# Performance work log

Measured on AMD Instinct MI355X. Metric: run time of the kernel, lower is better.

The kernel has to match this reference:

```python
import jax, jax.numpy as jnp
import numpy as np

NUM_HEADS = 16


def setup_inputs() -> dict:
    key = jax.random.key(0)
    ks = jax.random.split(key, 8)
    b, n, m, L, d = 2, 1024, 4, 1024, 1024
    x = jax.random.normal(ks[0], (b, n, d), dtype=jnp.float32)
    context = jax.random.normal(ks[1], (b, m, L, d), dtype=jnp.float32)
    doc_similarities = jax.random.normal(ks[2], (b, m), dtype=jnp.float32)
    mask = jnp.ones((b, n), dtype=bool)
    context_mask = jnp.ones((b, m, L), dtype=bool)
    Wq = jax.random.normal(ks[3], (d, d), dtype=jnp.float32) * 0.02
    Wkv = jax.random.normal(ks[4], (d, 2 * d), dtype=jnp.float32) * 0.02
    Wout = jax.random.normal(ks[5], (d, d), dtype=jnp.float32) * 0.02
    bout = jnp.zeros((d,), dtype=jnp.float32)
    beta = jnp.ones((), dtype=jnp.float32)
    return {"x": x, "context": context, "doc_similarities": doc_similarities,
            "mask": mask, "context_mask": context_mask,
            "Wq": Wq, "Wkv": Wkv, "Wout": Wout, "bout": bout, "beta": beta}


def reference(x, context, doc_similarities, mask, context_mask, Wq, Wkv, Wout, bout, beta):
    b, n, d = x.shape
    h = NUM_HEADS
    hd = d // h
    _, m, L, _ = context.shape
    kv_len = m * L

    # q projection -> (b, h, n, hd)
    q = (x @ Wq).reshape(b, n, h, hd).transpose(0, 2, 1, 3)

    ctx = context.reshape(b, kv_len, d)
    cmask = context_mask.reshape(b, kv_len)

    # doc similarity bias, broadcast per-token within each doc, scaled by beta
    ds = jnp.repeat(doc_similarities[:, :, None], L, axis=-1).reshape(b, kv_len)
    ds = ds[:, None, None, :] * beta  # (b, 1, 1, kv_len)

    kv = ctx @ Wkv  # (b, kv_len, 2d)
    k, v = jnp.split(kv, 2, axis=-1)
    k = k.reshape(b, kv_len, h, hd).transpose(0, 2, 3, 1)  # (b, h, hd, kv_len)
    v = v.reshape(b, kv_len, h, hd).transpose(0, 2, 1, 3)  # (b, h, kv_len, hd)

    # NOTE: original scales by d**-0.5 (full model dim), not head_size**-0.5
    attention_pre_doc_sim = (q @ k) * (d ** -0.5)  # (b, h, n, kv_len)
    attention = attention_pre_doc_sim + ds

    # faithful mask path: multiply by cross mask, then map exact zeros to -inf
    cross_mask = mask[:, None, :, None] * cmask[:, None, None, :]  # (b,1,n,kv_len)
    attention = attention * cross_mask
    attention = jnp.where(attention == 0.0, -jnp.inf, attention)

    attention_weights = jax.nn.softmax(attention, axis=-1)
    # dropout_rate = 0.0 -> identity

    out = (attention_weights @ v).transpose(0, 2, 1, 3).reshape(b, n, d)
    out = out @ Wout + bout
    return out, attention_pre_doc_sim
```

## Files before the change

kernel.cpp:

```cpp
#include <hip/hip_runtime.h>
#include <cstdint>
#include <cstddef>

typedef unsigned short u16t;
typedef __attribute__((ext_vector_type(4))) float f32x4;
typedef __attribute__((ext_vector_type(4))) int i32x4;
typedef __attribute__((ext_vector_type(4))) unsigned int u32x4;
typedef __attribute__((ext_vector_type(8))) __bf16 bf16x8;
typedef __attribute__((ext_vector_type(4))) __bf16 bf16x4;
typedef __attribute__((ext_vector_type(8))) unsigned short u16x8;
typedef __attribute__((ext_vector_type(4))) unsigned short u16x4;

#define INFF __builtin_inff()

__device__ __forceinline__ u16t f2b(float f) {
  union { float f; unsigned u; } x; x.f = f;
  unsigned r = x.u + 0x7FFFu + ((x.u >> 16) & 1u);
  return (u16t)(r >> 16);
}

__device__ __forceinline__ void gload16(const u16t* g, u16t* l) {
  __builtin_amdgcn_global_load_lds((const __attribute__((address_space(1))) void*)g,
                                   (__attribute__((address_space(3))) void*)l, 16, 0, 0);
}

__global__ __launch_bounds__(256) void k_prep(const float* __restrict__ x,
                                              const float* __restrict__ ctx,
                                              u16t* __restrict__ x16,
                                              u16t* __restrict__ ctx16,
                                              const int* __restrict__ cmask,
                                              unsigned int* __restrict__ cmbits) {
  const int bx = blockIdx.x, tid = threadIdx.x;
  if (bx < 2048) {
    int i = bx * 256 + tid;
    f32x4 v = *(const f32x4*)(x + (size_t)i * 4);
    u16x4 o;
    o[0] = f2b(v[0]); o[1] = f2b(v[1]); o[2] = f2b(v[2]); o[3] = f2b(v[3]);
    *(u16x4*)(x16 + (size_t)i * 4) = o;
  } else if (bx < 10240) {
    int i = (bx - 2048) * 256 + tid;
    f32x4 v = *(const f32x4*)(ctx + (size_t)i * 4);
    u16x4 o;
    o[0] = f2b(v[0]); o[1] = f2b(v[1]); o[2] = f2b(v[2]); o[3] = f2b(v[3]);
    *(u16x4*)(ctx16 + (size_t)i * 4) = o;
  } else {
    int b = tid >> 7, wdi = tid & 127;
    const int* cp = cmask + b * 4096 + wdi * 32;
    unsigned int bits = 0;
#pragma unroll
    for (int i = 0; i < 32; ++i) bits |= (cp[i] != 0 ? 1u : 0u) << i;
    cmbits[tid] = bits;
  }
}

__global__ __launch_bounds__(256) void k_transpose_w3(const float* __restrict__ Wq,
                                                      const float* __restrict__ Wkv,
                                                      const float* __restrict__ Wout,
                                                      u16t* __restrict__ WqT,
                                                      u16t* __restrict__ WkvT,
                                                      u16t* __restrict__ WoutT) {
  __shared__ float tile[64 * 65];
  const int t = threadIdx.x;
  const int bxx = blockIdx.x;
  const float* src; u16t* dst; int C, cb;
  if (bxx < 16)      { src = Wq;   dst = WqT;   C = 1024; cb = bxx * 64; }
  else if (bxx < 48) { src = Wkv;  dst = WkvT;  C = 2048; cb = (bxx - 16) * 64; }
  else               { src = Wout; dst = WoutT; C = 1024; cb = (bxx - 48) * 64; }
  const int rb = blockIdx.y * 64;
#pragma unroll
  for (int it = 0; it < 4; ++it) {
    int c = it * 256 + t;
    int r = c >> 4, ch = c & 15;
    f32x4 v = *(const f32x4*)(src + (size_t)(rb + r) * C + cb + ch * 4);
    float* dp = &tile[r * 65 + ch * 4];
    dp[0] = v[0]; dp[1] = v[1]; dp[2] = v[2]; dp[3] = v[3];
  }
  __syncthreads();
#pragma unroll
  for (int it = 0; it < 2; ++it) {
    int c = it * 256 + t;
    int dr = c >> 3, ch = c & 7;
    u16x8 o;
#pragma unroll
    for (int i = 0; i < 8; ++i) o[i] = f2b(tile[(ch * 8 + i) * 65 + dr]);
    *(u16x8*)(dst + (size_t)(cb + dr) * 1024 + rb + ch * 8) = o;
  }
}

template <int MODE>
__global__ __launch_bounds__(256) void k_gemm_bt(const u16t* __restrict__ A,
                                                 const u16t* __restrict__ Bt,
                                                 void* __restrict__ C,
                                                 u16t* __restrict__ C2,
                                                 const float* __restrict__ bias,
                                                 float oscale,
                                                 int K, int lda, int ldb, int ldc, int nbx) {
  __shared__ u16t As[128 * 64];
  __shared__ u16t Bs[128 * 64];
  const int tid = threadIdx.x;
  const int lane = tid & 63, wid = tid >> 6;
  const int l16 = lane & 15, lg = lane >> 4;
  const int wr = wid >> 1, wc = wid & 1;
  const int g = blockIdx.x, per = gridDim.x >> 3;
  const int w = (g & 7) * per + (g >> 3);
  const int bx = w % nbx, by = w / nbx;
  const int brow = by * 128, bcol = bx * 128;
  const int sr = lane >> 3, chs = lane & 7;
  f32x4 acc[4][4] = {};

  for (int k0 = 0; k0 < K; k0 += 64) {
#pragma unroll
    for (int it = 0; it < 4; ++it) {
      int row = it * 32 + wid * 8 + sr;
      int ch = chs ^ (row & 7);
      gload16(A + (size_t)(brow + row) * lda + k0 + ch * 8, &As[it * 2048 + wid * 512]);
      gload16(Bt + (size_t)(bcol + row) * ldb + k0 + ch * 8, &Bs[it * 2048 + wid * 512]);
    }
    __syncthreads();
#pragma unroll
    for (int kk = 0; kk < 2; ++kk) {
      bf16x8 af[4], bfv[4];
#pragma unroll
      for (int mi = 0; mi < 4; ++mi) {
        int row = wr * 64 + mi * 16 + l16;
        int kch = (kk * 4 + lg) ^ (row & 7);
        af[mi] = *(const bf16x8*)(&As[row * 64 + kch * 8]);
      }
#pragma unroll
      for (int ni = 0; ni < 4; ++ni) {
        int row = wc * 64 + ni * 16 + l16;
        int kch = (kk * 4 + lg) ^ (row & 7);
        bfv[ni] = *(const bf16x8*)(&Bs[row * 64 + kch * 8]);
      }
#pragma unroll
      for (int mi = 0; mi < 4; ++mi)
#pragma unroll
        for (int ni = 0; ni < 4; ++ni)
          acc[mi][ni] = __builtin_amdgcn_mfma_f32_16x16x32_bf16(af[mi], bfv[ni], acc[mi][ni], 0, 0, 0);
    }
    __syncthreads();
  }

  if (MODE == 2 && bcol >= 1024) {
#pragma unroll
    for (int mi = 0; mi < 4; ++mi) {
#pragma unroll
      for (int ni = 0; ni < 4; ++ni) {
        int vcol = bcol - 1024 + wc * 64 + ni * 16 + l16;
        int h = vcol >> 6, hd = vcol & 63;
        int row0 = brow + wr * 64 + mi * 16 + lg * 4;
        int bb = row0 >> 12, pos = row0 & 4095;
        u16x4 o4;
#pragma unroll
        for (int j = 0; j < 4; ++j) o4[j] = f2b(acc[mi][ni][j]);
        *(u16x4*)(C2 + ((size_t)((bb * 16 + h) * 64 + hd)) * 4096 + pos) = o4;
      }
    }
    return;
  }
#pragma unroll
  for (int mi = 0; mi < 4; ++mi) {
#pragma unroll
    for (int ni = 0; ni < 4; ++ni) {
#pragma unroll
      for (int j = 0; j < 4; ++j) {
        size_t row = (size_t)brow + wr * 64 + mi * 16 + lg * 4 + j;
        int col = bcol + wc * 64 + ni * 16 + l16;
        float v = acc[mi][ni][j] * oscale;
        if (MODE == 1) {
          v += bias[col];
          __builtin_nontemporal_store(v, (float*)C + row * ldc + col);
        } else {
          ((u16t*)C)[row * ldc + col] = f2b(v);
        }
      }
    }
  }
}

__global__ __launch_bounds__(256) void k_attn(const u16t* __restrict__ k16,
                                              const u16t* __restrict__ vT16,
                                              const u16t* __restrict__ q16,
                                              const unsigned int* __restrict__ cmbits,
                                              const float* __restrict__ dsim,
                                              const float* __restrict__ beta_p,
                                              const int* __restrict__ mask,
                                              float* __restrict__ pre,
                                              u16t* __restrict__ O16) {
  __shared__ u16t Ks[2][128 * 64];
  __shared__ u16t Vs[2][64 * 128];
  __shared__ u16t Ps[4 * 16 * 128];

  const int tid = threadIdx.x;
  const int lane = tid & 63, wid = tid >> 6;
  const int l16 = lane & 15, lg = lane >> 4;
  const int g = blockIdx.x;
  const int w = (g & 7) * 64 + (g >> 3);
  const int nb = w & 15, hb = w >> 4;
  const int h = hb & 15, b = hb >> 4;
  const int qrow0 = nb * 64 + wid * 16;

  bf16x8 aq0, aq1;
  {
    const u16t* qp = q16 + (size_t)(b * 1024 + qrow0 + l16) * 1024 + h * 64 + lg * 8;
    aq0 = *(const bf16x8*)(qp);
    aq1 = *(const bf16x8*)(qp + 32);
  }
  const bool qm = mask[b * 1024 + qrow0 + l16] != 0;

  const float beta = beta_p[0];
  const float ds40 = dsim[b * 4 + 0] * beta, ds41 = dsim[b * 4 + 1] * beta;
  const float ds42 = dsim[b * 4 + 2] * beta, ds43 = dsim[b * 4 + 3] * beta;

  float mrow = -INFF, lsum = 0.f;
  f32x4 o[4] = {};

  const u16t* kbase = k16 + (size_t)b * 4096 * 1024 + (size_t)h * 64;
  const u16t* vbase = vT16 + (size_t)(b * 16 + h) * 64 * 4096;
  float* prerow = pre + (size_t)((b * 16 + h) * 1024 + qrow0 + l16) * 4096;
  const u32x4* cmw = (const u32x4*)(cmbits + b * 128);
  u16t* Pw = &Ps[wid * 2048];
  char* Pwb = (char*)Pw + l16 * 256;
  const int pswz = (l16 & 7) << 4;

  auto stage = [&](int bufi, int kv0s) {
    u16t* Kb = &Ks[bufi][wid * 2048];
    u16t* Vb = &Vs[bufi][wid * 2048];
#pragma unroll
    for (int it = 0; it < 4; ++it) {
      int row = wid * 32 + it * 8 + (lane >> 3);
      int ch = (lane & 7) ^ (row & 7);
      gload16(kbase + (size_t)(kv0s + row) * 1024 + ch * 8, Kb + it * 512);
    }
#pragma unroll
    for (int it = 0; it < 4; ++it) {
      int row = wid * 16 + it * 4 + (lane >> 4);
      int ch = (lane & 15) ^ (row & 7);
      gload16(vbase + (size_t)row * 4096 + kv0s + ch * 8, Vb + it * 512);
    }
  };

  u32x4 Wc = cmw[0];
  int cur = 0;
  stage(0, 0);
  __syncthreads();

  for (int t = 0; t < 32; ++t) {
    u32x4 Wn = Wc;
    if (t + 1 < 32) {
      Wn = cmw[t + 1];
      stage(cur ^ 1, (t + 1) * 128);
    }
    asm volatile("" ::: "memory");
    const u16t* Kc = &Ks[cur][0];
    const u16t* Vc = &Vs[cur][0];
    const int kv0 = t * 128;
    const int d = t >> 3;
    const float ds_t = (d & 1) ? ((d & 2) ? ds43 : ds41) : ((d & 2) ? ds42 : ds40);

    f32x4 s[8];
#pragma unroll
    for (int kb = 0; kb < 8; ++kb) {
      f32x4 acc = {0.f, 0.f, 0.f, 0.f};
      int row = kb * 16 + l16;
      bf16x8 bk0 = *(const bf16x8*)(&Kc[row * 64 + ((lg ^ (row & 7)) << 3)]);
      bf16x8 bk1 = *(const bf16x8*)(&Kc[row * 64 + (((4 + lg) ^ (row & 7)) << 3)]);
      acc = __builtin_amdgcn_mfma_f32_16x16x32_bf16(bk0, aq0, acc, 0, 0, 0);
      acc = __builtin_amdgcn_mfma_f32_16x16x32_bf16(bk1, aq1, acc, 0, 0, 0);
      s[kb] = acc;
    }

    float tmax = -INFF;
#pragma unroll
    for (int kb = 0; kb < 8; ++kb) {
      const int colb = kv0 + kb * 16 + lg * 4;
      __builtin_nontemporal_store(s[kb], (f32x4*)(prerow + colb));
      const unsigned int sh = Wc[kb >> 1] >> ((kb & 1) * 16 + lg * 4);
#pragma unroll
      for (int j = 0; j < 4; ++j) {
        float bias = ((sh >> j) & 1u) ? ds_t : -INFF;
        float t2 = s[kb][j] + bias;
        if (!qm) t2 = 0.f;
        if (t2 == 0.f) t2 = -INFF;
        s[kb][j] = t2;
        tmax = fmaxf(tmax, t2);
      }
    }
    tmax = fmaxf(tmax, __shfl_xor(tmax, 16, 64));
    tmax = fmaxf(tmax, __shfl_xor(tmax, 32, 64));
    const float mold = mrow;
    const float mn = fmaxf(mold, tmax);
    const bool nochange = __all(mn == mold);
    mrow = mn;

    float psum = 0.f;
#pragma unroll
    for (int kb = 0; kb < 8; ++kb) {
      bf16x4 pb;
#pragma unroll
      for (int j = 0; j < 4; ++j) {
        float p = (mn == -INFF) ? 0.f : __expf(s[kb][j] - mn);
        psum += p;
        pb[j] = (__bf16)p;
      }
      *(bf16x4*)(Pwb + ((kb * 32 + lg * 8) ^ pswz)) = pb;
    }
    asm volatile("" ::: "memory");
    psum += __shfl_xor(psum, 16, 64);
    psum += __shfl_xor(psum, 32, 64);

    if (nochange) {
      lsum += psum;
    } else {
      const float fs = (mn == -INFF) ? 0.f : __expf(mold - mn);
      lsum = lsum * fs + psum;
      float fsj[4];
#pragma unroll
      for (int j = 0; j < 4; ++j) fsj[j] = __shfl(fs, lg * 4 + j, 64);
#pragma unroll
      for (int ni = 0; ni < 4; ++ni)
#pragma unroll
        for (int j = 0; j < 4; ++j) o[ni][j] *= fsj[j];
    }

#pragma unroll
    for (int kk2 = 0; kk2 < 4; ++kk2) {
      bf16x8 pa = *(const bf16x8*)(Pwb + ((kk2 * 64 + lg * 16) ^ pswz));
#pragma unroll
      for (int ni = 0; ni < 4; ++ni) {
        int vrow = ni * 16 + l16;
        bf16x8 vb = *(const bf16x8*)(&Vc[vrow * 128 + (((kk2 * 4 + lg) ^ (vrow & 7)) << 3)]);
        o[ni] = __builtin_amdgcn_mfma_f32_16x16x32_bf16(pa, vb, o[ni], 0, 0, 0);
      }
    }

    asm volatile("s_waitcnt vmcnt(8) lgkmcnt(0)" ::: "memory");
    __builtin_amdgcn_sched_barrier(0);
    __builtin_amdgcn_s_barrier();
    __builtin_amdgcn_sched_barrier(0);
    Wc = Wn;
    cur ^= 1;
  }

  float lsj[4];
#pragma unroll
  for (int j = 0; j < 4; ++j) lsj[j] = __shfl(lsum, lg * 4 + j, 64);
#pragma unroll
  for (int ni = 0; ni < 4; ++ni) {
#pragma unroll
    for (int j = 0; j < 4; ++j) {
      size_t row = (size_t)b * 1024 + qrow0 + lg * 4 + j;
      int col = h * 64 + ni * 16 + l16;
      O16[row * 1024 + col] = f2b(o[ni][j] / lsj[j]);
    }
  }
}

extern "C" void kernel_launch(void* const* d_in, const int* in_sizes, int n_in,
                              void* d_out, int out_size, void* d_ws, size_t ws_size,
                              hipStream_t stream) {
  const float* x = (const float*)d_in[0];
  const float* ctx = (const float*)d_in[1];
  const float* dsim = (const float*)d_in[2];
  const int* mask = (const int*)d_in[3];
  const int* cmask = (const int*)d_in[4];
  const float* Wq = (const float*)d_in[5];
  const float* Wkv = (const float*)d_in[6];
  const float* Wout = (const float*)d_in[7];
  const float* bout = (const float*)d_in[8];
  const float* beta = (const float*)d_in[9];

  char* ws = (char*)d_ws;
  u16t* q16 = (u16t*)(ws + (0ull << 20));
  u16t* k16 = (u16t*)(ws + (4ull << 20));
  u16t* vT16 = (u16t*)(ws + (36ull << 20));
  u16t* O16 = (u16t*)(ws + (52ull << 20));
  u16t* x16 = (u16t*)(ws + (56ull << 20));
  u16t* ctx16 = (u16t*)(ws + (60ull << 20));
  u16t* WqT = (u16t*)(ws + (76ull << 20));
  u16t* WkvT = (u16t*)(ws + (78ull << 20));
  u16t* WoutT = (u16t*)(ws + (82ull << 20));
  unsigned int* cmbits = (unsigned int*)(ws + (84ull << 20));

  float* outp = (float*)d_out;
  float* pre = outp + (size_t)2 * 1024 * 1024;

  k_prep<<<10241, 256, 0, stream>>>(x, ctx, x16, ctx16, cmask, cmbits);
  k_transpose_w3<<<dim3(64, 16), 256, 0, stream>>>(Wq, Wkv, Wout, WqT, WkvT, WoutT);

  k_gemm_bt<0><<<128, 256, 0, stream>>>(x16, WqT, (void*)q16, nullptr, nullptr, 0.03125f, 1024, 1024, 1024, 1024, 8);
  k_gemm_bt<2><<<1024, 256, 0, stream>>>(ctx16, WkvT, (void*)k16, vT16, nullptr, 1.0f, 1024, 1024, 1024, 1024, 16);
  k_attn<<<512, 256, 0, stream>>>(k16, vT16, q16, cmbits, dsim, beta, mask, pre, O16);
  k_gemm_bt<1><<<128, 256, 0, stream>>>(O16, WoutT, d_out, nullptr, bout, 1.0f, 1024, 1024, 1024, 1024, 8);
}
```

Measured before the change: 263.4 us.

## Load K/V directly from global and coalesce pre-score stores via LDS staging

Removes the double-buffered LDS staging of K and V tiles and the per-iteration block barrier. Each wave now reads K and V fragments straight from global memory, relying on the cache. The raw scores are written to a swizzled per-wave LDS buffer and then stored to the pre-softmax output as full contiguous row segments rather than scattered 16-byte fragments. s_setprio is also raised around the MFMA sections. The trade-off is losing explicit prefetch overlap and shared K/V reuse across waves, in exchange for better-coalesced writes of the large fp32 score tensor and no block synchronisation.

Result: slower. 349.2 us (+32.6%).

```diff
diff --git a/kernel.cpp b/kernel.cpp
--- a/kernel.cpp
+++ b/kernel.cpp
@@ -187,9 +187,8 @@
                                               const int* __restrict__ mask,
                                               float* __restrict__ pre,
                                               u16t* __restrict__ O16) {
-  __shared__ u16t Ks[2][128 * 64];
-  __shared__ u16t Vs[2][64 * 128];
-  __shared__ u16t Ps[4 * 16 * 128];
+  __shared__ u16t Ps[4 * 2048];
+  __shared__ float Sf[4 * 2048];
 
   const int tid = threadIdx.x;
   const int lane = tid & 63, wid = tid >> 6;
@@ -217,64 +216,38 @@
 
   const u16t* kbase = k16 + (size_t)b * 4096 * 1024 + (size_t)h * 64;
   const u16t* vbase = vT16 + (size_t)(b * 16 + h) * 64 * 4096;
-  float* prerow = pre + (size_t)((b * 16 + h) * 1024 + qrow0 + l16) * 4096;
+  float* preb = pre + (size_t)((b * 16 + h) * 1024 + qrow0) * 4096;
   const u32x4* cmw = (const u32x4*)(cmbits + b * 128);
-  u16t* Pw = &Ps[wid * 2048];
-  char* Pwb = (char*)Pw + l16 * 256;
+  char* Pwb = (char*)&Ps[wid * 2048] + l16 * 256;
   const int pswz = (l16 & 7) << 4;
-
-  auto stage = [&](int bufi, int kv0s) {
-    u16t* Kb = &Ks[bufi][wid * 2048];
-    u16t* Vb = &Vs[bufi][wid * 2048];
-#pragma unroll
-    for (int it = 0; it < 4; ++it) {
-      int row = wid * 32 + it * 8 + (lane >> 3);
-      int ch = (lane & 7) ^ (row & 7);
-      gload16(kbase + (size_t)(kv0s + row) * 1024 + ch * 8, Kb + it * 512);
-    }
-#pragma unroll
-    for (int it = 0; it < 4; ++it) {
-      int row = wid * 16 + it * 4 + (lane >> 4);
-      int ch = (lane & 15) ^ (row & 7);
-      gload16(vbase + (size_t)row * 4096 + kv0s + ch * 8, Vb + it * 512);
-    }
-  };
-
-  u32x4 Wc = cmw[0];
-  int cur = 0;
-  stage(0, 0);
-  __syncthreads();
+  char* Swave = (char*)&Sf[wid * 2048];
+  char* Swb = Swave + l16 * 512;
 
   for (int t = 0; t < 32; ++t) {
-    u32x4 Wn = Wc;
-    if (t + 1 < 32) {
-      Wn = cmw[t + 1];
-      stage(cur ^ 1, (t + 1) * 128);
-    }
-    asm volatile("" ::: "memory");
-    const u16t* Kc = &Ks[cur][0];
-    const u16t* Vc = &Vs[cur][0];
     const int kv0 = t * 128;
+    const u32x4 Wc = cmw[t];
     const int d = t >> 3;
     const float ds_t = (d & 1) ? ((d & 2) ? ds43 : ds41) : ((d & 2) ? ds42 : ds40);
+    const u16t* kt = kbase + (size_t)kv0 * 1024;
 
     f32x4 s[8];
+    __builtin_amdgcn_s_setprio(1);
 #pragma unroll
     for (int kb = 0; kb < 8; ++kb) {
+      const u16t* kr = kt + (size_t)(kb * 16 + l16) * 1024 + lg * 8;
+      bf16x8 bk0 = *(const bf16x8*)(kr);
+      bf16x8 bk1 = *(const bf16x8*)(kr + 32);
       f32x4 acc = {0.f, 0.f, 0.f, 0.f};
-      int row = kb * 16 + l16;
-      bf16x8 bk0 = *(const bf16x8*)(&Kc[row * 64 + ((lg ^ (row & 7)) << 3)]);
-      bf16x8 bk1 = *(const bf16x8*)(&Kc[row * 64 + (((4 + lg) ^ (row & 7)) << 3)]);
       acc = __builtin_amdgcn_mfma_f32_16x16x32_bf16(bk0, aq0, acc, 0, 0, 0);
       acc = __builtin_amdgcn_mfma_f32_16x16x32_bf16(bk1, aq1, acc, 0, 0, 0);
       s[kb] = acc;
     }
+    __builtin_amdgcn_s_setprio(0);
 
     float tmax = -INFF;
 #pragma unroll
     for (int kb = 0; kb < 8; ++kb) {
-      const int colb = kv0 + kb * 16 + lg * 4;
-      __builtin_nontemporal_store(s[kb], (f32x4*)(prerow + colb));
+      *(f32x4*)(Swb + ((kb * 64 + lg * 16) ^ pswz)) = s[kb];
       const unsigned int sh = Wc[kb >> 1] >> ((kb & 1) * 16 + lg * 4);
 #pragma unroll
       for (int j = 0; j < 4; ++j) {
@@ -323,23 +296,26 @@
         for (int j = 0; j < 4; ++j) o[ni][j] *= fsj[j];
     }
 
+    __builtin_amdgcn_s_setprio(1);
 #pragma unroll
     for (int kk2 = 0; kk2 < 4; ++kk2) {
       bf16x8 pa = *(const bf16x8*)(Pwb + ((kk2 * 64 + lg * 16) ^ pswz));
 #pragma unroll
       for (int ni = 0; ni < 4; ++ni) {
-        int vrow = ni * 16 + l16;
-        bf16x8 vb = *(const bf16x8*)(&Vc[vrow * 128 + (((kk2 * 4 + lg) ^ (vrow & 7)) << 3)]);
+        bf16x8 vb = *(const bf16x8*)(vbase + (size_t)(ni * 16 + l16) * 4096 + kv0 + kk2 * 32 + lg * 8);
         o[ni] = __builtin_amdgcn_mfma_f32_16x16x32_bf16(pa, vb, o[ni], 0, 0, 0);
       }
     }
-
-    asm volatile("s_waitcnt vmcnt(8) lgkmcnt(0)" ::: "memory");
-    __builtin_amdgcn_sched_barrier(0);
-    __builtin_amdgcn_s_barrier();
-    __builtin_amdgcn_sched_barrier(0);
-    Wc = Wn;
-    cur ^= 1;
+    __builtin_amdgcn_s_setprio(0);
+
+    asm volatile("" ::: "memory");
+    const int rhalf = lane >> 5, c4 = (lane & 31) * 4;
+#pragma unroll
+    for (int i = 0; i < 8; ++i) {
+      const int row2 = i * 2 + rhalf;
+      f32x4 v = *(const f32x4*)(Swave + row2 * 512 + ((c4 * 4) ^ ((row2 & 7) << 4)));
+      __builtin_nontemporal_store(v, (f32x4*)(preb + (size_t)row2 * 4096 + kv0 + c4));
+    }
   }
 
   float lsj[4];
```
